# Kernel optimization log

Hardware: AMD Instinct MI355X
Metric: run time of the kernel (lower is better)

The kernel has to match this reference:

```python
import jax, jax.numpy as jnp
import numpy as np

B, N, D = 2, 8192, 1024
H, Dh = 16, 64
P = H * Dh
EPS = 1e-6
DECAY_BIAS_SHIFT = 2.0


def setup_inputs() -> dict:
    key = jax.random.key(0)
    ks = jax.random.split(key, 7)
    s_in = 1.0 / np.sqrt(D)
    s_out = 1.0 / np.sqrt(P)
    return {
        "x": jax.random.normal(ks[0], (B, N, D), jnp.float32),
        "Wq": jax.random.normal(ks[1], (D, P), jnp.float32) * s_in,
        "Wk": jax.random.normal(ks[2], (D, P), jnp.float32) * s_in,
        "Wv": jax.random.normal(ks[3], (D, P), jnp.float32) * s_in,
        "Wo": jax.random.normal(ks[4], (P, D), jnp.float32) * s_out,
        "Wa": jax.random.normal(ks[5], (D, H), jnp.float32) * s_in,
        "ba": jnp.zeros((H,), jnp.float32),
    }


def _elu_plus_one(x):
    return jax.nn.elu(x) + 1.0


def _ssd_scan(q, k, v, a, eps):
    # q,k,v: (B,H,N,Dh); a: (B,H,N) in (0,1)
    # Recurrence: S_t = a_t*S_{t-1} + k_t v_t^T ; z_t = a_t*z_{t-1} + k_t
    # out_t = (q_t @ S_t) / (q_t . z_t + eps)
    qT = jnp.moveaxis(q, 2, 0)  # (N,B,H,Dh)
    kT = jnp.moveaxis(k, 2, 0)
    vT = jnp.moveaxis(v, 2, 0)
    aT = jnp.moveaxis(a, 2, 0)  # (N,B,H)

    Bb, Hh, _, Dk = q.shape
    Dv = v.shape[-1]
    S0 = jnp.zeros((Bb, Hh, Dk, Dv), q.dtype)
    z0 = jnp.zeros((Bb, Hh, Dk), q.dtype)

    def step(carry, inp):
        S, z = carry
        qt, kt, vt, at = inp
        S = at[..., None, None] * S + kt[..., :, None] * vt[..., None, :]
        z = at[..., None] * z + kt
        num = jnp.einsum("bhk,bhkv->bhv", qt, S)
        den = jnp.einsum("bhk,bhk->bh", qt, z) + eps
        return (S, z), num / den[..., None]

    _, outT = jax.lax.scan(step, (S0, z0), (qT, kT, vT, aT))
    return jnp.moveaxis(outT, 0, 2)  # (B,H,N,Dv)


def reference(x, Wq, Wk, Wv, Wo, Wa, ba):
    b, n, _ = x.shape
    q = (x @ Wq).reshape(b, n, H, Dh).transpose(0, 2, 1, 3)
    k = (x @ Wk).reshape(b, n, H, Dh).transpose(0, 2, 1, 3)
    v = (x @ Wv).reshape(b, n, H, Dh).transpose(0, 2, 1, 3)
    q = _elu_plus_one(q)
    k = _elu_plus_one(k)
    a = jax.nn.sigmoid(x @ Wa + ba + DECAY_BIAS_SHIFT)  # (B,N,H)
    a = a.transpose(0, 2, 1)  # (B,H,N)
    out = _ssd_scan(q, k, v, a, EPS)  # (B,H,N,Dh)
    out = out.transpose(0, 2, 1, 3).reshape(b, n, P)
    return out @ Wo
```

## Files before the change

### kernel.cpp

```cpp
#include <hip/hip_runtime.h>
#include <stdint.h>

#define HH 16
#define DH 64
#define DD 1024
#define PP 1024
#define NNLEN 8192
#define BBATCH 2
#define MM (BBATCH*NNLEN)
#define CCHUNK 128
#define LCH 64
#define NGRP 16
#define GCH 8
#define EPSV 1e-6f

typedef unsigned short u16;
typedef __attribute__((ext_vector_type(4))) unsigned short u16x4;
typedef __attribute__((ext_vector_type(8))) unsigned short u16x8;
typedef __attribute__((ext_vector_type(8))) __bf16 bf16x8;
typedef __attribute__((ext_vector_type(4))) float f32x4;

__device__ __forceinline__ u16 f2bf(float f) {
  unsigned x = __float_as_uint(f);
  return (u16)((x + 0x7fffu + ((x >> 16) & 1u)) >> 16);
}
__device__ __forceinline__ float bf2f(u16 u) {
  return __uint_as_float(((unsigned)u) << 16);
}

__device__ __forceinline__ void gl2lds16(const void* g, void* l) {
  __builtin_amdgcn_global_load_lds(
      reinterpret_cast<__attribute__((address_space(1))) void*>(
          reinterpret_cast<uintptr_t>(g)),
      reinterpret_cast<__attribute__((address_space(3))) void*>(
          reinterpret_cast<uintptr_t>(l)),
      16, 0, 0);
}

__device__ __forceinline__ bf16x8 ldsw(const u16* base, int row, int col) {
  union { u16x8 u; bf16x8 b; } cv;
  cv.u = *(const u16x8*)&base[row * 64 + (col ^ ((row & 7) << 3))];
  return cv.b;
}

__device__ __forceinline__ bf16x8 ldsw32(const u16* base, int row, int col) {
  union { u16x8 u; bf16x8 b; } cv;
  cv.u = *(const u16x8*)&base[row * 32 + (col ^ (((row >> 1) & 3) << 3))];
  return cv.b;
}

__global__ __launch_bounds__(256)
void prep_all(const float* __restrict__ x, u16* __restrict__ xb,
              const float* __restrict__ Wq, u16* __restrict__ WqT,
              const float* __restrict__ Wk, u16* __restrict__ WkT,
              const float* __restrict__ Wv, u16* __restrict__ WvT,
              const float* __restrict__ Wo, u16* __restrict__ WoT,
              const float* __restrict__ Wa, u16* __restrict__ WaT) {
  __shared__ float tile[32][33];
  const int bid = blockIdx.x;
  const int tid = threadIdx.x;
  if (bid < 8192) {
    size_t i = ((size_t)bid * 256 + tid) * 8;
    f32x4 a = *(const f32x4*)(x + i);
    f32x4 b = *(const f32x4*)(x + i + 4);
    u16x8 o;
    o[0] = f2bf(a[0]); o[1] = f2bf(a[1]); o[2] = f2bf(a[2]); o[3] = f2bf(a[3]);
    o[4] = f2bf(b[0]); o[5] = f2bf(b[1]); o[6] = f2bf(b[2]); o[7] = f2bf(b[3]);
    *(u16x8*)(xb + i) = o;
    return;
  }
  if (bid < 12288) {
    const int t = (bid - 8192) >> 10;
    const int sub = (bid - 8192) & 1023;
    const float* in = (t == 0) ? Wq : (t == 1) ? Wk : (t == 2) ? Wv : Wo;
    u16* out = (t == 0) ? WqT : (t == 1) ? WkT : (t == 2) ? WvT : WoT;
    const int bx = (sub & 31) * 32, by = (sub >> 5) * 32;
    const int tx = tid & 31, ty = tid >> 5;
    for (int i2 = ty; i2 < 32; i2 += 8)
      tile[i2][tx] = in[(size_t)(by + i2) * 1024 + bx + tx];
    __syncthreads();
    for (int i2 = ty; i2 < 32; i2 += 8)
      out[(size_t)(bx + i2) * 1024 + by + tx] = f2bf(tile[tx][i2]);
    return;
  }
  {
    int idx = (bid - 12288) * 256 + tid;
    WaT[idx] = f2bf(Wa[(idx & 1023) * 16 + (idx >> 10)]);
  }
}

__global__ __launch_bounds__(256)
void a_proj(const u16* __restrict__ xb, const u16* __restrict__ WaT,
            const float* __restrict__ ba, float* __restrict__ abuf) {
  __shared__ __align__(16) u16 As[256 * 32];
  __shared__ __align__(16) u16 Bs[16 * 32];
  const int tid = threadIdx.x;
  const int brow = blockIdx.x * 256;
  const int l = tid & 63, wid = tid >> 6;
  const int la = l & 15, kb8 = (l >> 4) * 8;
  const int sr = tid >> 2, se = (tid & 3) * 8;

  f32x4 acc[4];
#pragma unroll
  for (int mi = 0; mi < 4; ++mi) acc[mi] = (f32x4){0.f, 0.f, 0.f, 0.f};

  for (int kt = 0; kt < 32; ++kt) {
    const int k0 = kt * 32;
    __syncthreads();
#pragma unroll
    for (int i = 0; i < 4; ++i)
      gl2lds16(xb + (size_t)(brow + i * 64 + sr) * DD + k0 + se,
               &As[i * 2048 + wid * 512]);
    if (wid == 0)
      gl2lds16(WaT + (size_t)(l >> 2) * DD + k0 + (l & 3) * 8, &Bs[0]);
    __syncthreads();
    union { u16x8 u; bf16x8 b; } cvb;
    cvb.u = *(const u16x8*)&Bs[la * 32 + kb8];
#pragma unroll
    for (int mi = 0; mi < 4; ++mi) {
      union { u16x8 u; bf16x8 b; } cva;
      cva.u = *(const u16x8*)&As[(wid * 64 + mi * 16 + la) * 32 + kb8];
      acc[mi] = __builtin_amdgcn_mfma_f32_16x16x32_bf16(cva.b, cvb.b, acc[mi], 0, 0, 0);
    }
  }
  const float bav = ba[la];
#pragma unroll
  for (int mi = 0; mi < 4; ++mi)
#pragma unroll
    for (int rr = 0; rr < 4; ++rr) {
      int row = brow + wid * 64 + mi * 16 + ((l >> 4) << 2) + rr;
      float t = acc[mi][rr] + bav + 2.0f;
      abuf[(size_t)row * HH + la] = 1.f / (1.f + __expf(-t));
    }
}

template<int NCT, int ROUTE>
__global__ __launch_bounds__(512, 4)
void gemm_tb(const u16* __restrict__ A, const u16* __restrict__ Bt,
             void* __restrict__ Cout) {
  __shared__ __align__(16) u16 As[2][256 * 32];
  __shared__ __align__(16) u16 Bs[2][128 * 32];
  const int tid = threadIdx.x;
  const int nwg = gridDim.x;
  const int f = blockIdx.x;
  const int swz = (f & 7) * (nwg >> 3) + (f >> 3);
  const int brow = (swz / NCT) * 256;
  const int bcol = (swz % NCT) * 128;
  const int l = tid & 63;
  const int wid = tid >> 6;
  const int wrow = (wid >> 1) * 64;
  const int wcol = (wid & 1) * 64;
  const int la = l & 15, kb8 = (l >> 4) * 8;
  const int K = 1024;
  const int srow = l >> 2;
  const int scol = (((l & 3) ^ ((l >> 3) & 3)) << 3);

  f32x4 acc[4][4];
#pragma unroll
  for (int i = 0; i < 4; ++i)
#pragma unroll
    for (int j = 0; j < 4; ++j) acc[i][j] = (f32x4){0.f, 0.f, 0.f, 0.f};

#pragma unroll
  for (int j = 0; j < 2; ++j) {
    const int r0 = (wid * 2 + j) * 16 + srow;
    gl2lds16(A + (size_t)(brow + r0) * K + scol, &As[0][(wid * 2 + j) * 512]);
  }
  gl2lds16(Bt + (size_t)(bcol + wid * 16 + srow) * K + scol, &Bs[0][wid * 512]);
  asm volatile("s_waitcnt vmcnt(0)" ::: "memory");
  __builtin_amdgcn_s_barrier();

  const int NKT = K / 32;
  for (int kt = 0; kt < NKT; ++kt) {
    const u16* lA = As[kt & 1];
    const u16* lB = Bs[kt & 1];
    u16* nA = As[(kt + 1) & 1];
    u16* nB = Bs[(kt + 1) & 1];
    const int knext = (kt + 1) * 32;
    const bool more = (kt + 1 < NKT);

    if (more) {
#pragma unroll
      for (int j = 0; j < 2; ++j) {
        const int r0 = (wid * 2 + j) * 16 + srow;
        gl2lds16(A + (size_t)(brow + r0) * K + knext + scol,
                 nA + (wid * 2 + j) * 512);
      }
      gl2lds16(Bt + (size_t)(bcol + wid * 16 + srow) * K + knext + scol,
               nB + wid * 512);
    }

    bf16x8 bfr[4];
#pragma unroll
    for (int n2 = 0; n2 < 4; ++n2)
      bfr[n2] = ldsw32(lB, wcol + n2 * 16 + la, kb8);

    __builtin_amdgcn_s_setprio(1);
#pragma unroll
    for (int m2 = 0; m2 < 4; ++m2) {
      bf16x8 afm = ldsw32(lA, wrow + m2 * 16 + la, kb8);
#pragma unroll
      for (int n2 = 0; n2 < 4; ++n2)
        acc[m2][n2] = __builtin_amdgcn_mfma_f32_16x16x32_bf16(
            afm, bfr[n2], acc[m2][n2], 0, 0, 0);
    }
    __builtin_amdgcn_s_setprio(0);

    if (more) {
      asm volatile("s_waitcnt vmcnt(0)" ::: "memory");
      __builtin_amdgcn_s_barrier();
    }
  }

  if (ROUTE) {
    u16* base = (u16*)Cout + (size_t)(bcol >> 10) * ((size_t)MM * 1024);
    const bool act = (bcol < 2048);
#pragma unroll
    for (int mi = 0; mi < 4; ++mi)
#pragma unroll
      for (int ni = 0; ni < 4; ++ni)
#pragma unroll
        for (int rr = 0; rr < 4; ++rr) {
          int row = brow + wrow + mi * 16 + ((l >> 4) << 2) + rr;
          int c2 = (bcol & 1023) + wcol + ni * 16 + la;
          float v = acc[mi][ni][rr];
          if (act) v = v > 0.f ? v + 1.f : __expf(v);
          base[(size_t)row * 1024 + c2] = f2bf(v);
        }
  } else {
#pragma unroll
    for (int mi = 0; mi < 4; ++mi)
#pragma unroll
      for (int ni = 0; ni < 4; ++ni)
#pragma unroll
        for (int rr = 0; rr < 4; ++rr) {
          int row = brow + wrow + mi * 16 + ((l >> 4) << 2) + rr;
          int col = bcol + wcol + ni * 16 + la;
          ((float*)Cout)[(size_t)row * 1024 + col] = acc[mi][ni][rr];
        }
  }
}

__global__ __launch_bounds__(256)
void chunk_local_scan(const u16* __restrict__ kb, const u16* __restrict__ vb,
                      const float* __restrict__ abuf,
                      u16* __restrict__ Sbuf, float* __restrict__ zbuf,
                      float* __restrict__ cAbuf,
                      float* __restrict__ GAgg, float* __restrict__ zGAgg,
                      float* __restrict__ dpbuf) {
  const int g = blockIdx.x & (NGRP - 1);
  const int bh = blockIdx.x >> 4;
  const int h = bh & (HH - 1);
  const int b = bh >> 4;
  __shared__ __align__(16) u16 KT[64 * 64];
  __shared__ __align__(16) u16 VTl[64 * 64];
  __shared__ float wshA[GCH][64];
  __shared__ float dchA[GCH];
  const int tid = threadIdx.x;
  const int r = tid >> 2, e = (tid & 3) * 16;
  const int l = tid & 63, w = tid >> 6;
  const int kb8 = (l >> 4) << 3, la = l & 15;
  const int dw = 16 * w + ((l >> 4) << 2);
  const int dkz = tid >> 2, tqz = (tid & 3) * 16, swkz = (dkz & 7) << 3;
  const int c0 = g * GCH;
  const int rowbase0 = b * NNLEN + c0 * LCH;

#pragma unroll
  for (int ii = 0; ii < 2; ++ii) {
    const int i = w * 2 + ii;
    const int blkc = bh * CCHUNK + c0 + i;
    float v = __logf(abuf[(size_t)(rowbase0 + i * LCH + l) * HH + h]);
#pragma unroll
    for (int d = 1; d < 64; d <<= 1) {
      float u = __shfl_up(v, d);
      if (l >= d) v += u;
    }
    cAbuf[(size_t)blkc * 64 + l] = v;
    float tot = __shfl(v, 63);
    wshA[i][l] = __expf(tot - v);
    if (l == 0) dchA[i] = __expf(tot);
  }
  __syncthreads();
  if (tid == 0) {
    float rp = 1.f;
#pragma unroll
    for (int i = 0; i < GCH; ++i) {
      dpbuf[bh * CCHUNK + c0 + i] = rp;
      rp *= dchA[i];
    }
  }

  f32x4 run[4];
#pragma unroll
  for (int ni = 0; ni < 4; ++ni) run[ni] = (f32x4){0.f, 0.f, 0.f, 0.f};
  float zrun = 0.f;

  const u16* kp = kb + (size_t)(rowbase0 + r) * PP + h * DH + e;
  const u16* vp = vb + (size_t)(rowbase0 + r) * PP + h * DH + e;
  u16x8 k0 = *(const u16x8*)kp, k1 = *(const u16x8*)(kp + 8);
  u16x8 v0 = *(const u16x8*)vp, v1 = *(const u16x8*)(vp + 8);

  for (int i = 0; i < GCH; ++i) {
    const int blkc = bh * CCHUNK + c0 + i;
    if (i) __syncthreads();

    {
      const float wt = wshA[i][r];
#pragma unroll
      for (int j = 0; j < 8; ++j) {
        int d0 = e + j, d1 = e + 8 + j;
        KT[d0 * 64 + (r ^ ((d0 & 7) << 3))] = f2bf(bf2f(k0[j]) * wt);
        KT[d1 * 64 + (r ^ ((d1 & 7) << 3))] = f2bf(bf2f(k1[j]) * wt);
        VTl[d0 * 64 + (r ^ ((d0 & 7) << 3))] = v0[j];
        VTl[d1 * 64 + (r ^ ((d1 & 7) << 3))] = v1[j];
      }
    }
    __syncthreads();

    if (i + 1 < GCH) {
      const int rb = rowbase0 + (i + 1) * LCH;
      kp = kb + (size_t)(rb + r) * PP + h * DH + e;
      vp = vb + (size_t)(rb + r) * PP + h * DH + e;
      k0 = *(const u16x8*)kp; k1 = *(const u16x8*)(kp + 8);
      v0 = *(const u16x8*)vp; v1 = *(const u16x8*)(vp + 8);
    }

    const float dch = dchA[i];
    f32x4 s[4];
#pragma unroll
    for (int ni = 0; ni < 4; ++ni) s[ni] = (f32x4){0.f, 0.f, 0.f, 0.f};
#pragma unroll
    for (int kk = 0; kk < 2; ++kk) {
      bf16x8 av = ldsw(VTl, 16 * w + la, kk * 32 + kb8);
#pragma unroll
      for (int ni = 0; ni < 4; ++ni)
        s[ni] = __builtin_amdgcn_mfma_f32_16x16x32_bf16(
            av, ldsw(KT, 16 * ni + la, kk * 32 + kb8), s[ni], 0, 0, 0);
    }

    u16* Sc = Sbuf + (size_t)blkc * 4096;
#pragma unroll
    for (int ni = 0; ni < 4; ++ni)
#pragma unroll
      for (int rr = 0; rr < 4; ++rr)
        Sc[(dw + rr) * 64 + 16 * ni + la] = f2bf(run[ni][rr]);
#pragma unroll
    for (int ni = 0; ni < 4; ++ni)
#pragma unroll
      for (int rr = 0; rr < 4; ++rr)
        run[ni][rr] = dch * run[ni][rr] + s[ni][rr];

    {
      float zp = 0.f;
#pragma unroll
      for (int i2 = 0; i2 < 16; ++i2)
        zp += bf2f(KT[dkz * 64 + ((tqz + i2) ^ swkz)]);
      zp += __shfl_xor(zp, 1);
      zp += __shfl_xor(zp, 2);
      if ((tid & 3) == 0) zbuf[(size_t)blkc * 64 + dkz] = zrun;
      zrun = dch * zrun + zp;
    }
  }

  float* Ga = GAgg + ((size_t)bh * NGRP + g) * 4096;
#pragma unroll
  for (int ni = 0; ni < 4; ++ni)
#pragma unroll
    for (int rr = 0; rr < 4; ++rr)
      Ga[(dw + rr) * 64 + 16 * ni + la] = run[ni][rr];
  if ((tid & 3) == 0)
    zGAgg[((size_t)bh * NGRP + g) * 64 + dkz] = zrun;
}

__global__ __launch_bounds__(1024)
void scan_top(const float* __restrict__ GAgg, u16* __restrict__ GBeg,
              float* __restrict__ zGAgg, const float* __restrict__ cAbuf) {
  const int bh = blockIdx.x;
  const size_t cb = (size_t)bh * CCHUNK;
  __shared__ float Dsh[NGRP];
  if (threadIdx.x < NGRP) {
    float s = 0.f;
#pragma unroll
    for (int i = 0; i < GCH; ++i)
      s += cAbuf[(cb + threadIdx.x * GCH + i) * 64 + 63];
    Dsh[threadIdx.x] = __expf(s);
  }
  __syncthreads();
  const int elem = threadIdx.x * 4;
  const float* base = GAgg + (size_t)bh * NGRP * 4096;
  u16* gb = GBeg + (size_t)bh * NGRP * 4096;
  f32x4 run = (f32x4){0.f, 0.f, 0.f, 0.f};
  f32x4 cur = *(const f32x4*)&base[elem];
#pragma unroll
  for (int gg = 0; gg < NGRP; ++gg) {
    f32x4 nxt;
    if (gg + 1 < NGRP) nxt = *(const f32x4*)&base[(gg + 1) * 4096 + elem];
    u16x4 o;
#pragma unroll
    for (int jj = 0; jj < 4; ++jj) o[jj] = f2bf(run[jj]);
    *(u16x4*)&gb[gg * 4096 + elem] = o;
    const float D = Dsh[gg];
#pragma unroll
    for (int jj = 0; jj < 4; ++jj) run[jj] = D * run[jj] + cur[jj];
    cur = nxt;
  }
  if (threadIdx.x < 64) {
    float* zb = zGAgg + (size_t)bh * NGRP * 64;
    float zr = 0.f;
#pragma unroll
    for (int gg = 0; gg < NGRP; ++gg) {
      float a = zb[gg * 64 + threadIdx.x];
      zb[gg * 64 + threadIdx.x] = zr;
      zr = Dsh[gg] * zr + a;
    }
  }
}

__global__ __launch_bounds__(256)
void chunk_out(u16* __restrict__ qb, const u16* __restrict__ kb,
               const u16* __restrict__ vb, const u16* __restrict__ Sbuf,
               const float* __restrict__ zbuf, const float* __restrict__ cAbuf,
               const u16* __restrict__ GBeg, const float* __restrict__ zGAgg,
               const float* __restrict__ dpbuf) {
  const int blk = blockIdx.x;
  const int c = blk & (CCHUNK - 1);
  const int h = (blk >> 7) & (HH - 1);
  const int b = blk >> 11;
  const int bh = blk >> 7;
  const int g = c >> 3;
  const int rowbase = b * NNLEN + c * LCH;

  __shared__ __align__(16) u16 Qs[64 * 64];
  __shared__ __align__(16) u16 Ke[64 * 64];
  __shared__ __align__(16) u16 VT[64 * 64];
  __shared__ __align__(16) u16 STs[64 * 64];
  __shared__ float cAsh[64], zsh[64], denP[64], qzs[64];

  const int tid = threadIdx.x;
  const int r = tid >> 2, e = (tid & 3) * 16;
  const float dp = dpbuf[blk];

  const u16* qp = qb + (size_t)(rowbase + r) * PP + h * DH + e;
  const u16* kp = kb + (size_t)(rowbase + r) * PP + h * DH + e;
  const u16* vp = vb + (size_t)(rowbase + r) * PP + h * DH + e;
  u16x8 q0 = *(const u16x8*)qp, q1 = *(const u16x8*)(qp + 8);
  u16x8 k0 = *(const u16x8*)kp, k1 = *(const u16x8*)(kp + 8);
  u16x8 v0 = *(const u16x8*)vp, v1 = *(const u16x8*)(vp + 8);
  const u16* sp = Sbuf + (size_t)blk * 4096 + r * 64 + e;
  u16x8 p0 = *(const u16x8*)sp, p1 = *(const u16x8*)(sp + 8);
  const u16* gp = GBeg + ((size_t)bh * NGRP + g) * 4096 + r * 64 + e;
  u16x8 gb0 = *(const u16x8*)gp, gb1 = *(const u16x8*)(gp + 8);
  if (tid < 64) {
    cAsh[tid] = cAbuf[(size_t)blk * 64 + tid];
    zsh[tid] = zbuf[(size_t)blk * 64 + tid]
             + dp * zGAgg[((size_t)bh * NGRP + g) * 64 + tid];
  }
  __syncthreads();

  {
    const float c0c = cAsh[31];
    const int sw = (r & 7) << 3;
    const float qsc = __expf(cAsh[r] - c0c);
    const float ksc = __expf(c0c - cAsh[r]);
    const float ssc = __expf(c0c);
    u16x8 t0, t1, u0, u1, w0, w1;
#pragma unroll
    for (int j = 0; j < 8; ++j) {
      t0[j] = f2bf(bf2f(q0[j]) * qsc);
      t1[j] = f2bf(bf2f(q1[j]) * qsc);
      u0[j] = f2bf(bf2f(k0[j]) * ksc);
      u1[j] = f2bf(bf2f(k1[j]) * ksc);
    }
#pragma unroll
    for (int j = 0; j < 8; ++j) {
      w0[j] = f2bf((bf2f(p0[j]) + dp * bf2f(gb0[j])) * ssc);
      w1[j] = f2bf((bf2f(p1[j]) + dp * bf2f(gb1[j])) * ssc);
    }
    *(u16x8*)&Qs[r * 64 + (e ^ sw)] = t0;
    *(u16x8*)&Qs[r * 64 + ((e + 8) ^ sw)] = t1;
    *(u16x8*)&Ke[r * 64 + (e ^ sw)] = u0;
    *(u16x8*)&Ke[r * 64 + ((e + 8) ^ sw)] = u1;
    *(u16x8*)&STs[r * 64 + (e ^ sw)] = w0;
    *(u16x8*)&STs[r * 64 + ((e + 8) ^ sw)] = w1;
#pragma unroll
    for (int j = 0; j < 8; ++j) {
      int d0 = e + j, d1 = e + 8 + j;
      VT[d0 * 64 + (r ^ ((d0 & 7) << 3))] = v0[j];
      VT[d1 * 64 + (r ^ ((d1 & 7) << 3))] = v1[j];
    }
    if (tid < 64) zsh[tid] *= ssc;
  }
  __syncthreads();

  const int l = tid & 63, w = tid >> 6;
  const int kb8 = (l >> 4) << 3, la = l & 15;

  bf16x8 aq[2];
  f32x4 p[4];
#pragma unroll
  for (int ni = 0; ni < 4; ++ni) p[ni] = (f32x4){0.f, 0.f, 0.f, 0.f};
#pragma unroll
  for (int kk = 0; kk < 2; ++kk) {
    aq[kk] = ldsw(Qs, 16 * w + la, kk * 32 + kb8);
#pragma unroll
    for (int ni = 0; ni < 4; ++ni)
      p[ni] = __builtin_amdgcn_mfma_f32_16x16x32_bf16(
          aq[kk], ldsw(Ke, 16 * ni + la, kk * 32 + kb8), p[ni], 0, 0, 0);
  }

  const int tw = 16 * w + ((l >> 4) << 2);
  float rsum[4] = {0.f, 0.f, 0.f, 0.f};
#pragma unroll
  for (int ni = 0; ni < 4; ++ni)
#pragma unroll
    for (int rr = 0; rr < 4; ++rr) {
      int s = 16 * ni + la, t = tw + rr;
      float v = (s <= t) ? p[ni][rr] : 0.f;
      p[ni][rr] = v;
      rsum[rr] += v;
    }
#pragma unroll
  for (int d = 1; d < 16; d <<= 1)
#pragma unroll
    for (int rr = 0; rr < 4; ++rr) rsum[rr] += __shfl_xor(rsum[rr], d);
  if (la == 0)
#pragma unroll
    for (int rr = 0; rr < 4; ++rr) denP[tw + rr] = rsum[rr];

  {
    float qzp = 0.f;
#pragma unroll
    for (int kk = 0; kk < 2; ++kk)
#pragma unroll
      for (int j = 0; j < 8; ++j) {
        union { bf16x8 b; u16x8 u; } cv; cv.b = aq[kk];
        qzp += bf2f(cv.u[j]) * zsh[kk * 32 + kb8 + j];
      }
    qzp += __shfl_xor(qzp, 16);
    qzp += __shfl_xor(qzp, 32);
    if (l < 16) qzs[16 * w + la] = qzp;
  }
  __syncthreads();

#pragma unroll
  for (int ni = 0; ni < 4; ++ni)
#pragma unroll
    for (int rr = 0; rr < 4; ++rr) {
      int t = tw + rr, s = 16 * ni + la;
      Ke[t * 64 + (s ^ ((t & 7) << 3))] = f2bf(p[ni][rr]);
    }
  __syncthreads();

  f32x4 o[4];
#pragma unroll
  for (int ni = 0; ni < 4; ++ni) o[ni] = (f32x4){0.f, 0.f, 0.f, 0.f};
#pragma unroll
  for (int kk = 0; kk < 2; ++kk) {
    bf16x8 ap = ldsw(Ke, 16 * w + la, kk * 32 + kb8);
#pragma unroll
    for (int ni = 0; ni < 4; ++ni)
      o[ni] = __builtin_amdgcn_mfma_f32_16x16x32_bf16(
          ap, ldsw(VT, 16 * ni + la, kk * 32 + kb8), o[ni], 0, 0, 0);
  }
#pragma unroll
  for (int kk = 0; kk < 2; ++kk)
#pragma unroll
    for (int ni = 0; ni < 4; ++ni)
      o[ni] = __builtin_amdgcn_mfma_f32_16x16x32_bf16(
          aq[kk], ldsw(STs, 16 * ni + la, kk * 32 + kb8), o[ni], 0, 0, 0);

  float dn[4];
#pragma unroll
  for (int rr = 0; rr < 4; ++rr) dn[rr] = qzs[tw + rr] + denP[tw + rr] + EPSV;
#pragma unroll
  for (int ni = 0; ni < 4; ++ni)
#pragma unroll
    for (int rr = 0; rr < 4; ++rr) {
      int t = tw + rr, dv = 16 * ni + la;
      qb[(size_t)(rowbase + t) * PP + h * DH + dv] = f2bf(o[ni][rr] / dn[rr]);
    }
}

extern "C" void kernel_launch(void* const* d_in, const int* in_sizes, int n_in,
                              void* d_out, int out_size, void* d_ws, size_t ws_size,
                              hipStream_t stream) {
  const float* x  = (const float*)d_in[0];
  const float* Wq = (const float*)d_in[1];
  const float* Wk = (const float*)d_in[2];
  const float* Wv = (const float*)d_in[3];
  const float* Wo = (const float*)d_in[4];
  const float* Wa = (const float*)d_in[5];
  const float* ba = (const float*)d_in[6];

  char* ws = (char*)d_ws;
  size_t off = 0;
  auto carve = [&](size_t bytes) {
    void* p = ws + off;
    off += (bytes + 255) & ~(size_t)255;
    return p;
  };
  u16* xb   = (u16*)carve((size_t)MM * DD * 2);
  u16* WqT  = (u16*)carve((size_t)PP * DD * 2);
  u16* WkT  = (u16*)carve((size_t)PP * DD * 2);
  u16* WvT  = (u16*)carve((size_t)PP * DD * 2);
  u16* WoT  = (u16*)carve((size_t)DD * PP * 2);
  u16* WaT  = (u16*)carve((size_t)HH * DD * 2);
  u16* qb   = (u16*)carve((size_t)MM * PP * 2);
  u16* kb   = (u16*)carve((size_t)MM * PP * 2);
  u16* vb   = (u16*)carve((size_t)MM * PP * 2);
  float* abuf  = (float*)carve((size_t)MM * HH * 4);
  u16*  Sbuf   = (u16*)carve((size_t)BBATCH * HH * CCHUNK * 4096 * 2);
  float* zbuf  = (float*)carve((size_t)BBATCH * HH * CCHUNK * 64 * 4);
  float* cAbuf = (float*)carve((size_t)BBATCH * HH * CCHUNK * 64 * 4);
  float* GAgg  = (float*)carve((size_t)BBATCH * HH * NGRP * 4096 * 4);
  u16*  GBeg   = (u16*)carve((size_t)BBATCH * HH * NGRP * 4096 * 2);
  float* zGAgg = (float*)carve((size_t)BBATCH * HH * NGRP * 64 * 4);
  float* dpbuf = (float*)carve((size_t)BBATCH * HH * CCHUNK * 4);

  prep_all<<<12352, 256, 0, stream>>>(x, xb, Wq, WqT, Wk, WkT, Wv, WvT,
                                      Wo, WoT, Wa, WaT);
  a_proj<<<MM / 256, 256, 0, stream>>>(xb, WaT, ba, abuf);

  gemm_tb<24, 1><<<(MM / 256) * 24, 512, 0, stream>>>(xb, WqT, qb);

  chunk_local_scan<<<BBATCH * HH * NGRP, 256, 0, stream>>>(
      kb, vb, abuf, Sbuf, zbuf, cAbuf, GAgg, zGAgg, dpbuf);
  scan_top<<<BBATCH * HH, 1024, 0, stream>>>(GAgg, GBeg, zGAgg, cAbuf);
  chunk_out<<<BBATCH * HH * CCHUNK, 256, 0, stream>>>(qb, kb, vb, Sbuf, zbuf, cAbuf,
                                                      GBeg, zGAgg, dpbuf);

  gemm_tb<8, 0><<<(MM / 256) * 8, 512, 0, stream>>>(qb, WoT, (float*)d_out);
}
```

Baseline: 264.7 us.

## Replace GEMM with 256x256 tile, BK=64, four-phase pipelined staging

The bf16 GEMM kernel used for the QKV projection and the output projection is rewritten. Tiles grow from 256x128 to 256x256 with a K-step of 64, and each of the 8 waves now owns a 128x64 sub-tile. Each K-iteration is split into four quadrant phases that interleave LDS fragment reads, async global-to-LDS staging of half-tiles and MFMA bursts, with partial vmcnt waits. This aims to raise arithmetic intensity and hide load latency. In exchange it uses double the registers and 128KB of LDS, drops the occupancy hint, and adds more barriers per iteration.

After: 258.4 us. 2.4% less time.

```diff
diff --git a/kernel.cpp b/kernel.cpp
--- a/kernel.cpp
+++ b/kernel.cpp
@@ -40,12 +40,6 @@
 __device__ __forceinline__ bf16x8 ldsw(const u16* base, int row, int col) {
   union { u16x8 u; bf16x8 b; } cv;
   cv.u = *(const u16x8*)&base[row * 64 + (col ^ ((row & 7) << 3))];
-  return cv.b;
-}
-
-__device__ __forceinline__ bf16x8 ldsw32(const u16* base, int row, int col) {
-  union { u16x8 u; bf16x8 b; } cv;
-  cv.u = *(const u16x8*)&base[row * 32 + (col ^ (((row >> 1) & 3) << 3))];
   return cv.b;
 }
 
@@ -134,89 +128,136 @@
     }
 }
 
+#define MMA_Q(MIH, NIH) \
+  __builtin_amdgcn_s_setprio(1); \
+  _Pragma("unroll") \
+  for (int m2 = 0; m2 < 4; ++m2) \
+    _Pragma("unroll") \
+    for (int n2 = 0; n2 < 2; ++n2) \
+      _Pragma("unroll") \
+      for (int kk = 0; kk < 2; ++kk) \
+        acc[(MIH) * 4 + m2][(NIH) * 2 + n2] = \
+            __builtin_amdgcn_mfma_f32_16x16x32_bf16( \
+                af[m2][kk], bfr[n2][kk], \
+                acc[(MIH) * 4 + m2][(NIH) * 2 + n2], 0, 0, 0); \
+  __builtin_amdgcn_s_setprio(0);
+
+#define RD_A(LA, MIH) \
+  _Pragma("unroll") \
+  for (int m2 = 0; m2 < 4; ++m2) \
+    _Pragma("unroll") \
+    for (int kk = 0; kk < 2; ++kk) \
+      af[m2][kk] = ldsw(LA, wr * 128 + (MIH) * 64 + m2 * 16 + la, kk * 32 + kb8);
+
+#define RD_B(LB, NIH) \
+  _Pragma("unroll") \
+  for (int n2 = 0; n2 < 2; ++n2) \
+    _Pragma("unroll") \
+    for (int kk = 0; kk < 2; ++kk) \
+      bfr[n2][kk] = ldsw(LB, wc * 64 + (NIH) * 32 + n2 * 16 + la, kk * 32 + kb8);
+
+#define VMCNT(N) \
+  asm volatile("s_waitcnt vmcnt(" #N ")" ::: "memory"); \
+  __builtin_amdgcn_sched_barrier(0);
+
 template<int NCT, int ROUTE>
-__global__ __launch_bounds__(512, 4)
-void gemm_tb(const u16* __restrict__ A, const u16* __restrict__ Bt,
+__global__ __launch_bounds__(512)
+void gemm_4p(const u16* __restrict__ A, const u16* __restrict__ Bt,
              void* __restrict__ Cout) {
-  __shared__ __align__(16) u16 As[2][256 * 32];
-  __shared__ __align__(16) u16 Bs[2][128 * 32];
+  __shared__ __align__(16) u16 As[2][256 * 64];
+  __shared__ __align__(16) u16 Bs[2][256 * 64];
   const int tid = threadIdx.x;
   const int nwg = gridDim.x;
   const int f = blockIdx.x;
   const int swz = (f & 7) * (nwg >> 3) + (f >> 3);
   const int brow = (swz / NCT) * 256;
-  const int bcol = (swz % NCT) * 128;
+  const int bcol = (swz % NCT) * 256;
   const int l = tid & 63;
   const int wid = tid >> 6;
-  const int wrow = (wid >> 1) * 64;
-  const int wcol = (wid & 1) * 64;
+  const int wr = wid >> 2;
+  const int wc = wid & 3;
   const int la = l & 15, kb8 = (l >> 4) * 8;
   const int K = 1024;
-  const int srow = l >> 2;
-  const int scol = (((l & 3) ^ ((l >> 3) & 3)) << 3);
-
-  f32x4 acc[4][4];
-#pragma unroll
-  for (int i = 0; i < 4; ++i)
+  const int srow = l >> 3;
+  const int scol = ((l & 7) * 8) ^ (srow << 3);
+
+  auto stageA = [&](int H, int koff, u16* dst) {
+#pragma unroll
+    for (int j = 0; j < 2; ++j) {
+      const int i2 = wid * 2 + j;
+      const int chunk = (i2 < 8) ? (H * 8 + i2) : (16 + H * 8 + (i2 - 8));
+      gl2lds16(A + (size_t)(brow + chunk * 8 + srow) * K + koff + scol,
+               dst + chunk * 512);
+    }
+  };
+  auto stageB = [&](int H, int koff, u16* dst) {
+#pragma unroll
+    for (int j = 0; j < 2; ++j) {
+      const int i2 = wid * 2 + j;
+      const int chunk = (i2 >> 2) * 8 + H * 4 + (i2 & 3);
+      gl2lds16(Bt + (size_t)(bcol + chunk * 8 + srow) * K + koff + scol,
+               dst + chunk * 512);
+    }
+  };
+
+  f32x4 acc[8][4];
+#pragma unroll
+  for (int i = 0; i < 8; ++i)
 #pragma unroll
     for (int j = 0; j < 4; ++j) acc[i][j] = (f32x4){0.f, 0.f, 0.f, 0.f};
 
-#pragma unroll
-  for (int j = 0; j < 2; ++j) {
-    const int r0 = (wid * 2 + j) * 16 + srow;
-    gl2lds16(A + (size_t)(brow + r0) * K + scol, &As[0][(wid * 2 + j) * 512]);
-  }
-  gl2lds16(Bt + (size_t)(bcol + wid * 16 + srow) * K + scol, &Bs[0][wid * 512]);
-  asm volatile("s_waitcnt vmcnt(0)" ::: "memory");
+  stageA(0, 0, As[0]);
+  stageB(0, 0, Bs[0]);
+  stageB(1, 0, Bs[0]);
+  stageA(1, 0, As[0]);
+  VMCNT(4);
   __builtin_amdgcn_s_barrier();
 
-  const int NKT = K / 32;
+  const int NKT = K / 64;
+  bf16x8 af[4][2], bfr[2][2];
   for (int kt = 0; kt < NKT; ++kt) {
     const u16* lA = As[kt & 1];
     const u16* lB = Bs[kt & 1];
     u16* nA = As[(kt + 1) & 1];
     u16* nB = Bs[(kt + 1) & 1];
-    const int knext = (kt + 1) * 32;
+    const int kn = (kt + 1) * 64;
     const bool more = (kt + 1 < NKT);
 
-    if (more) {
-#pragma unroll
-      for (int j = 0; j < 2; ++j) {
-        const int r0 = (wid * 2 + j) * 16 + srow;
-        gl2lds16(A + (size_t)(brow + r0) * K + knext + scol,
-                 nA + (wid * 2 + j) * 512);
-      }
-      gl2lds16(Bt + (size_t)(bcol + wid * 16 + srow) * K + knext + scol,
-               nB + wid * 512);
-    }
-
-    bf16x8 bfr[4];
-#pragma unroll
-    for (int n2 = 0; n2 < 4; ++n2)
-      bfr[n2] = ldsw32(lB, wcol + n2 * 16 + la, kb8);
-
-    __builtin_amdgcn_s_setprio(1);
-#pragma unroll
-    for (int m2 = 0; m2 < 4; ++m2) {
-      bf16x8 afm = ldsw32(lA, wrow + m2 * 16 + la, kb8);
-#pragma unroll
-      for (int n2 = 0; n2 < 4; ++n2)
-        acc[m2][n2] = __builtin_amdgcn_mfma_f32_16x16x32_bf16(
-            afm, bfr[n2], acc[m2][n2], 0, 0, 0);
-    }
-    __builtin_amdgcn_s_setprio(0);
-
-    if (more) {
-      asm volatile("s_waitcnt vmcnt(0)" ::: "memory");
-      __builtin_amdgcn_s_barrier();
-    }
-  }
-
+    RD_A(lA, 0);
+    RD_B(lB, 0);
+    if (more) stageA(0, kn, nA);
+    __builtin_amdgcn_s_barrier();
+    MMA_Q(0, 0);
+    if (more) { VMCNT(4); } else { VMCNT(2); }
+    __builtin_amdgcn_s_barrier();
+
+    RD_B(lB, 1);
+    if (more) stageB(0, kn, nB);
+    __builtin_amdgcn_s_barrier();
+    MMA_Q(0, 1);
+    if (more) { VMCNT(4); } else { VMCNT(0); }
+    __builtin_amdgcn_s_barrier();
+
+    RD_A(lA, 1);
+    if (more) stageB(1, kn, nB);
+    __builtin_amdgcn_s_barrier();
+    MMA_Q(1, 1);
+    __builtin_amdgcn_s_barrier();
+
+    RD_B(lB, 0);
+    if (more) stageA(1, kn, nA);
+    __builtin_amdgcn_s_barrier();
+    MMA_Q(1, 0);
+    if (more) { VMCNT(4); }
+    __builtin_amdgcn_s_barrier();
+  }
+
+  const int wrow = wr * 128, wcol = wc * 64;
   if (ROUTE) {
     u16* base = (u16*)Cout + (size_t)(bcol >> 10) * ((size_t)MM * 1024);
     const bool act = (bcol < 2048);
 #pragma unroll
-    for (int mi = 0; mi < 4; ++mi)
+    for (int mi = 0; mi < 8; ++mi)
 #pragma unroll
       for (int ni = 0; ni < 4; ++ni)
 #pragma unroll
@@ -229,7 +270,7 @@
         }
   } else {
 #pragma unroll
-    for (int mi = 0; mi < 4; ++mi)
+    for (int mi = 0; mi < 8; ++mi)
 #pragma unroll
       for (int ni = 0; ni < 4; ++ni)
 #pragma unroll
@@ -621,7 +662,7 @@
                                       Wo, WoT, Wa, WaT);
   a_proj<<<MM / 256, 256, 0, stream>>>(xb, WaT, ba, abuf);
 
-  gemm_tb<24, 1><<<(MM / 256) * 24, 512, 0, stream>>>(xb, WqT, qb);
+  gemm_4p<12, 1><<<(MM / 256) * 12, 512, 0, stream>>>(xb, WqT, qb);
 
   chunk_local_scan<<<BBATCH * HH * NGRP, 256, 0, stream>>>(
       kb, vb, abuf, Sbuf, zbuf, cAbuf, GAgg, zGAgg, dpbuf);
@@ -629,5 +670,5 @@
   chunk_out<<<BBATCH * HH * CCHUNK, 256, 0, stream>>>(qb, kb, vb, Sbuf, zbuf, cAbuf,
                                                       GBeg, zGAgg, dpbuf);
 
-  gemm_tb<8, 0><<<(MM / 256) * 8, 512, 0, stream>>>(qb, WoT, (float*)d_out);
-}
+  gemm_4p<4, 0><<<(MM / 256) * 4, 512, 0, stream>>>(qb, WoT, (float*)d_out);
+}
```

## Enlarge GEMM tiles to 256x256 with 16 waves and 64-wide K steps

Applied to the files above, without the earlier changes.

Replaces the 256x128, 8-wave GEMM with a 256x256 block tile run by 16 waves (1024 threads). Each K iteration now covers 64 elements instead of 32, using the 64-column swizzled LDS layout. The larger tile raises operand reuse per global load and halves the number of K-loop barriers, aiming to cut memory traffic for the QKV and output projections. In exchange, LDS use per block grows to 128 KB, which limits each CU to one resident block and risks poorer latency hiding and tail-wave behaviour.

Measured after the change: 253.2 us. 4.3% less time.

```diff
diff --git a/kernel.cpp b/kernel.cpp
--- a/kernel.cpp
+++ b/kernel.cpp
@@ -40,12 +40,6 @@
 __device__ __forceinline__ bf16x8 ldsw(const u16* base, int row, int col) {
   union { u16x8 u; bf16x8 b; } cv;
   cv.u = *(const u16x8*)&base[row * 64 + (col ^ ((row & 7) << 3))];
-  return cv.b;
-}
-
-__device__ __forceinline__ bf16x8 ldsw32(const u16* base, int row, int col) {
-  union { u16x8 u; bf16x8 b; } cv;
-  cv.u = *(const u16x8*)&base[row * 32 + (col ^ (((row >> 1) & 3) << 3))];
   return cv.b;
 }
 
@@ -135,25 +129,26 @@
 }
 
 template<int NCT, int ROUTE>
-__global__ __launch_bounds__(512, 4)
-void gemm_tb(const u16* __restrict__ A, const u16* __restrict__ Bt,
-             void* __restrict__ Cout) {
-  __shared__ __align__(16) u16 As[2][256 * 32];
-  __shared__ __align__(16) u16 Bs[2][128 * 32];
+__global__ __launch_bounds__(1024, 4)
+void gemm16(const u16* __restrict__ A, const u16* __restrict__ Bt,
+            void* __restrict__ Cout) {
+  __shared__ __align__(16) u16 As[2][256 * 64];
+  __shared__ __align__(16) u16 Bs[2][256 * 64];
   const int tid = threadIdx.x;
   const int nwg = gridDim.x;
   const int f = blockIdx.x;
   const int swz = (f & 7) * (nwg >> 3) + (f >> 3);
   const int brow = (swz / NCT) * 256;
-  const int bcol = (swz % NCT) * 128;
+  const int bcol = (swz % NCT) * 256;
   const int l = tid & 63;
   const int wid = tid >> 6;
-  const int wrow = (wid >> 1) * 64;
-  const int wcol = (wid & 1) * 64;
+  const int wr = wid >> 2;
+  const int wc = wid & 3;
   const int la = l & 15, kb8 = (l >> 4) * 8;
   const int K = 1024;
-  const int srow = l >> 2;
-  const int scol = (((l & 3) ^ ((l >> 3) & 3)) << 3);
+  const int srow = l >> 3;
+  const int scol = ((l & 7) * 8) ^ (srow << 3);
+  const int ldso = (wid * 2) * 512;
 
   f32x4 acc[4][4];
 #pragma unroll
@@ -163,48 +158,54 @@
 
 #pragma unroll
   for (int j = 0; j < 2; ++j) {
-    const int r0 = (wid * 2 + j) * 16 + srow;
-    gl2lds16(A + (size_t)(brow + r0) * K + scol, &As[0][(wid * 2 + j) * 512]);
-  }
-  gl2lds16(Bt + (size_t)(bcol + wid * 16 + srow) * K + scol, &Bs[0][wid * 512]);
+    const int r0 = (wid * 2 + j) * 8 + srow;
+    gl2lds16(A  + (size_t)(brow + r0) * K + scol, &As[0][ldso + j * 512]);
+    gl2lds16(Bt + (size_t)(bcol + r0) * K + scol, &Bs[0][ldso + j * 512]);
+  }
   asm volatile("s_waitcnt vmcnt(0)" ::: "memory");
   __builtin_amdgcn_s_barrier();
 
-  const int NKT = K / 32;
+  const int NKT = K / 64;
   for (int kt = 0; kt < NKT; ++kt) {
     const u16* lA = As[kt & 1];
     const u16* lB = Bs[kt & 1];
     u16* nA = As[(kt + 1) & 1];
     u16* nB = Bs[(kt + 1) & 1];
-    const int knext = (kt + 1) * 32;
+    const int knext = (kt + 1) * 64;
     const bool more = (kt + 1 < NKT);
 
     if (more) {
 #pragma unroll
       for (int j = 0; j < 2; ++j) {
-        const int r0 = (wid * 2 + j) * 16 + srow;
-        gl2lds16(A + (size_t)(brow + r0) * K + knext + scol,
-                 nA + (wid * 2 + j) * 512);
+        const int r0 = (wid * 2 + j) * 8 + srow;
+        gl2lds16(A  + (size_t)(brow + r0) * K + knext + scol,
+                 nA + ldso + j * 512);
+        gl2lds16(Bt + (size_t)(bcol + r0) * K + knext + scol,
+                 nB + ldso + j * 512);
       }
-      gl2lds16(Bt + (size_t)(bcol + wid * 16 + srow) * K + knext + scol,
-               nB + wid * 512);
-    }
-
-    bf16x8 bfr[4];
+    }
+
+    bf16x8 bfr[4][2];
 #pragma unroll
     for (int n2 = 0; n2 < 4; ++n2)
-      bfr[n2] = ldsw32(lB, wcol + n2 * 16 + la, kb8);
-
-    __builtin_amdgcn_s_setprio(1);
+#pragma unroll
+      for (int kk = 0; kk < 2; ++kk)
+        bfr[n2][kk] = ldsw(lB, wc * 64 + n2 * 16 + la, kk * 32 + kb8);
+
 #pragma unroll
     for (int m2 = 0; m2 < 4; ++m2) {
-      bf16x8 afm = ldsw32(lA, wrow + m2 * 16 + la, kb8);
-#pragma unroll
-      for (int n2 = 0; n2 < 4; ++n2)
+      bf16x8 af0 = ldsw(lA, wr * 64 + m2 * 16 + la, kb8);
+      bf16x8 af1 = ldsw(lA, wr * 64 + m2 * 16 + la, 32 + kb8);
+      __builtin_amdgcn_s_setprio(1);
+#pragma unroll
+      for (int n2 = 0; n2 < 4; ++n2) {
         acc[m2][n2] = __builtin_amdgcn_mfma_f32_16x16x32_bf16(
-            afm, bfr[n2], acc[m2][n2], 0, 0, 0);
-    }
-    __builtin_amdgcn_s_setprio(0);
+            af0, bfr[n2][0], acc[m2][n2], 0, 0, 0);
+        acc[m2][n2] = __builtin_amdgcn_mfma_f32_16x16x32_bf16(
+            af1, bfr[n2][1], acc[m2][n2], 0, 0, 0);
+      }
+      __builtin_amdgcn_s_setprio(0);
+    }
 
     if (more) {
       asm volatile("s_waitcnt vmcnt(0)" ::: "memory");
@@ -212,6 +213,7 @@
     }
   }
 
+  const int wrow = wr * 64, wcol = wc * 64;
   if (ROUTE) {
     u16* base = (u16*)Cout + (size_t)(bcol >> 10) * ((size_t)MM * 1024);
     const bool act = (bcol < 2048);
@@ -621,7 +623,7 @@
                                       Wo, WoT, Wa, WaT);
   a_proj<<<MM / 256, 256, 0, stream>>>(xb, WaT, ba, abuf);
 
-  gemm_tb<24, 1><<<(MM / 256) * 24, 512, 0, stream>>>(xb, WqT, qb);
+  gemm16<12, 1><<<(MM / 256) * 12, 1024, 0, stream>>>(xb, WqT, qb);
 
   chunk_local_scan<<<BBATCH * HH * NGRP, 256, 0, stream>>>(
       kb, vb, abuf, Sbuf, zbuf, cAbuf, GAgg, zGAgg, dpbuf);
@@ -629,5 +631,5 @@
   chunk_out<<<BBATCH * HH * CCHUNK, 256, 0, stream>>>(qb, kb, vb, Sbuf, zbuf, cAbuf,
                                                       GBeg, zGAgg, dpbuf);
 
-  gemm_tb<8, 0><<<(MM / 256) * 8, 512, 0, stream>>>(qb, WoT, (float*)d_out);
-}
+  gemm16<4, 0><<<(MM / 256) * 4, 1024, 0, stream>>>(qb, WoT, (float*)d_out);
+}
```
